# Kernel optimization log

Measured on AMD Instinct MI355X. Metric: run time of the kernel, lower is better.

The kernel has to match this reference:

```python
import jax, jax.numpy as jnp
import numpy as np

B, T, D_MODEL = 2, 1024, 512
EXPAND = 2
D_INNER = D_MODEL * EXPAND
STATE = 16
K_CONV = 4


def setup_inputs() -> dict:
    key = jax.random.key(0)
    ks = jax.random.split(key, 10)
    sc = lambda k, shape: jax.random.normal(k, shape, jnp.float32) * 0.02
    return {
        "x": jax.random.normal(ks[0], (B, T, D_MODEL), jnp.float32),
        "ln_g": jnp.ones((D_MODEL,), jnp.float32),
        "ln_b": jnp.zeros((D_MODEL,), jnp.float32),
        "W_in": sc(ks[1], (2 * D_INNER, D_MODEL)),
        "conv_w": sc(ks[2], (D_INNER, 1, K_CONV)),
        "conv_b": jnp.zeros((D_INNER,), jnp.float32),
        "W_B": sc(ks[3], (STATE, D_INNER)),
        "W_C": sc(ks[4], (STATE, D_INNER)),
        "W_dt": sc(ks[5], (D_INNER, D_INNER)),
        "b_dt": jax.random.uniform(ks[6], (D_INNER,), jnp.float32, -4.0, -1.0),
        # log_A init: A_diag = -(n+1) from HiPPO, log(-A_diag) = log(n+1), broadcast over d_inner
        "log_A": jnp.broadcast_to(jnp.log(jnp.arange(1, STATE + 1, dtype=jnp.float32)), (D_INNER, STATE)),
        "W_out": sc(ks[7], (D_MODEL, D_INNER)),
    }


def _silu(v):
    return v * jax.nn.sigmoid(v)


def reference(x, ln_g, ln_b, W_in, conv_w, conv_b, W_B, W_C, W_dt, b_dt, log_A, W_out):
    residual = x
    # LayerNorm (biased variance, eps=1e-5)
    mu = x.mean(-1, keepdims=True)
    var = x.var(-1, keepdims=True)
    xn = (x - mu) * jax.lax.rsqrt(var + 1e-5) * ln_g + ln_b
    # input projection and gate split
    xz = xn @ W_in.T                      # (B,T,2*D_INNER)
    x_main, z = jnp.split(xz, 2, axis=-1)
    # depthwise causal conv1d (padding=3 then slice to T == left-pad 3)
    xc = jnp.transpose(x_main, (0, 2, 1))  # (B,D_INNER,T)
    xc = jax.lax.conv_general_dilated(
        xc, conv_w, window_strides=(1,), padding=[(K_CONV - 1, 0)],
        dimension_numbers=("NCH", "OIH", "NCH"), feature_group_count=D_INNER,
    ) + conv_b[None, :, None]
    x_main = _silu(jnp.transpose(xc, (0, 2, 1)))  # (B,T,D_INNER)
    # selective scan in fp32
    xf = x_main.astype(jnp.float32)
    Bt = xf @ W_B.T                        # (B,T,N)
    Ct = xf @ W_C.T                        # (B,T,N)
    dt = jax.nn.softplus(xf @ W_dt.T + b_dt)  # (B,T,D_INNER)
    A = -jnp.exp(log_A)                    # (D_INNER,N)
    dA = jnp.exp(A[None, None] * dt[..., None])              # (B,T,D_INNER,N)
    dBx = dt[..., None] * Bt[:, :, None, :] * xf[..., None]  # (B,T,D_INNER,N)

    def comb(c1, c2):
        a1, b1 = c1
        a2, b2 = c2
        return a1 * a2, a2 * b1 + b2

    _, h = jax.lax.associative_scan(comb, (dA, dBx), axis=1)  # h_t = dA_t*h_{t-1}+dBx_t
    y = (h * Ct[:, :, None, :]).sum(-1).astype(x.dtype)       # (B,T,D_INNER)
    out = (y * _silu(z)) @ W_out.T
    return residual + out
```

## Files before the change

kernel.cpp:

```cpp
#include <hip/hip_runtime.h>

#define T_SEQ 1024
#define DM 512
#define DI 1024
#define NS 16
#define NC 64
#define CL 16

typedef __attribute__((ext_vector_type(8))) short short8;
typedef __attribute__((ext_vector_type(4))) float f32x4;
typedef unsigned short u16;
typedef unsigned int u32;

__device__ inline float b2f(u16 u) {
    unsigned v = ((unsigned)u) << 16;
    return __builtin_bit_cast(float, v);
}
__device__ inline u16 f2b(float f) {
    unsigned u = __builtin_bit_cast(unsigned, f);
    u += 0x7fff + ((u >> 16) & 1);
    return (u16)(u >> 16);
}

__device__ inline void g2l16(const u16* g, short* l) {
    __builtin_amdgcn_global_load_lds((const __attribute__((address_space(1))) u32*)g,
                                     (__attribute__((address_space(3))) u32*)l, 16, 0, 0);
}

__global__ void cast_w(const float* __restrict__ Win, const float* __restrict__ Wdt,
                       const float* __restrict__ Wout, const float* __restrict__ Wb,
                       const float* __restrict__ Wc,
                       u16* __restrict__ oWin, u16* __restrict__ oWdt, u16* __restrict__ oWout,
                       u16* __restrict__ oWb, u16* __restrict__ oWc) {
    int i = blockIdx.x * 256 + threadIdx.x;
    const float* s; u16* d; int off;
    if (i < 262144)      { s = Win;  d = oWin;  off = i; }
    else if (i < 524288) { s = Wdt;  d = oWdt;  off = i - 262144; }
    else if (i < 655360) { s = Wout; d = oWout; off = i - 524288; }
    else if (i < 659456) { s = Wb;   d = oWb;   off = i - 655360; }
    else                 { s = Wc;   d = oWc;   off = i - 659456; }
    float4 v = ((const float4*)s)[off];
    d[off * 4 + 0] = f2b(v.x);
    d[off * 4 + 1] = f2b(v.y);
    d[off * 4 + 2] = f2b(v.z);
    d[off * 4 + 3] = f2b(v.w);
}

__global__ __launch_bounds__(256) void ln_k(const float* __restrict__ x, const float* __restrict__ g,
                                            const float* __restrict__ be, u16* __restrict__ xn) {
    int row = blockIdx.x, tid = threadIdx.x;
    float2 v = ((const float2*)(x + row * DM))[tid];
    float s = v.x + v.y, q = v.x * v.x + v.y * v.y;
    #pragma unroll
    for (int m = 1; m < 64; m <<= 1) { s += __shfl_xor(s, m); q += __shfl_xor(q, m); }
    __shared__ float ss[4], qq[4];
    if ((tid & 63) == 0) { ss[tid >> 6] = s; qq[tid >> 6] = q; }
    __syncthreads();
    s = ss[0] + ss[1] + ss[2] + ss[3];
    q = qq[0] + qq[1] + qq[2] + qq[3];
    float mu = s / DM;
    float var = q / DM - mu * mu;
    float rs = rsqrtf(var + 1e-5f);
    int c = tid * 2;
    xn[row * DM + c]     = f2b((v.x - mu) * rs * g[c] + be[c]);
    xn[row * DM + c + 1] = f2b((v.y - mu) * rs * g[c + 1] + be[c + 1]);
}

template<int BM, int BN, int NT, int EPI>
__global__ __launch_bounds__(256) void gemm_bt(const u16* __restrict__ A, int lda,
                                               const u16* __restrict__ Bw, int ldb,
                                               void* __restrict__ outp, int ldo,
                                               const float* __restrict__ extra) {
    __shared__ short a_sh[2][BM * 32];
    __shared__ short b_sh[2][BN * 32];
    constexpr int MI = BM / 32, NJ = BN / 32;
    int tid = threadIdx.x, w = tid >> 6, lane = tid & 63;
    int m0 = blockIdx.x * BM, n0 = blockIdx.y * BN;
    int wr = (w >> 1) * (BM / 2), wc = (w & 1) * (BN / 2);
    int lr = lane & 15, kg = lane >> 4;
    f32x4 acc[MI][NJ] = {};
    const u16* Abase = A + (size_t)m0 * lda;
    const u16* Bbase = Bw + (size_t)n0 * ldb;
    int srow = w * 16 + (lane >> 2);
    int sc0 = (lane & 3);

    auto stage = [&](int cur, int kt) {
        int k0 = kt * 32;
        #pragma unroll
        for (int r = 0; r < BM / 64; ++r) {
            int row = r * 64 + srow;
            int sc = sc0 ^ ((row >> 1) & 3);
            g2l16(Abase + (size_t)row * lda + k0 + sc * 8, &a_sh[cur][r * 2048 + w * 512 + lane * 8]);
        }
        #pragma unroll
        for (int r = 0; r < BN / 64; ++r) {
            int row = r * 64 + srow;
            int sc = sc0 ^ ((row >> 1) & 3);
            g2l16(Bbase + (size_t)row * ldb + k0 + sc * 8, &b_sh[cur][r * 2048 + w * 512 + lane * 8]);
        }
    };

    stage(0, 0);
    __syncthreads();
    int cur = 0;
    for (int t = 0; t < NT; ++t) {
        if (t + 1 < NT) stage(cur ^ 1, t + 1);
        short8 af[MI], bfr[NJ];
        #pragma unroll
        for (int i = 0; i < MI; ++i) {
            int row = wr + i * 16 + lr;
            af[i] = *(const short8*)&a_sh[cur][row * 32 + (kg ^ ((row >> 1) & 3)) * 8];
        }
        #pragma unroll
        for (int j = 0; j < NJ; ++j) {
            int row = wc + j * 16 + lr;
            bfr[j] = *(const short8*)&b_sh[cur][row * 32 + (kg ^ ((row >> 1) & 3)) * 8];
        }
        #pragma unroll
        for (int i = 0; i < MI; ++i)
            #pragma unroll
            for (int j = 0; j < NJ; ++j)
                acc[i][j] = __builtin_amdgcn_mfma_f32_16x16x32_bf16(af[i], bfr[j], acc[i][j], 0, 0, 0);
        __syncthreads();
        cur ^= 1;
    }

    int rb = (lane >> 4) * 4, cc = lane & 15;
    #pragma unroll
    for (int i = 0; i < MI; ++i) {
        #pragma unroll
        for (int j = 0; j < NJ; ++j) {
            #pragma unroll
            for (int r = 0; r < 4; ++r) {
                int row = m0 + wr + i * 16 + rb + r;
                int col = n0 + wc + j * 16 + cc;
                float v = acc[i][j][r];
                if (EPI == 0) {
                    ((u16*)outp)[(size_t)row * ldo + col] = f2b(v);
                } else if (EPI == 1) {
                    float xx = v + extra[col];
                    float sp = (xx > 20.f) ? xx : log1pf(__expf(xx));
                    ((u16*)outp)[(size_t)row * ldo + col] = f2b(sp);
                } else {
                    ((float*)outp)[(size_t)row * ldo + col] = v + extra[(size_t)row * ldo + col];
                }
            }
        }
    }
}

__global__ void conv_k(const u16* __restrict__ xz, const float* __restrict__ w,
                       const float* __restrict__ cb, u16* __restrict__ xf) {
    int idx = blockIdx.x * 256 + threadIdx.x;
    int d = idx & (DI - 1);
    int bt = idx >> 10;
    int t = bt & (T_SEQ - 1);
    float s = cb[d];
    #pragma unroll
    for (int i = 0; i < 4; ++i) {
        int tt = t - 3 + i;
        if (tt >= 0) s += w[d * 4 + i] * b2f(xz[(size_t)(bt - 3 + i) * 2048 + d]);
    }
    float sig = 1.f / (1.f + __expf(-s));
    xf[idx] = f2b(s * sig);
}

__global__ __launch_bounds__(256) void bc_k(const u16* __restrict__ xf, const u16* __restrict__ Wb,
                                            const u16* __restrict__ Wc,
                                            float* __restrict__ Bt, float* __restrict__ Ct) {
    int m = blockIdx.x * 8 + (threadIdx.x >> 5);
    int j = threadIdx.x & 31;
    const u16* wrow = (j < 16) ? (Wb + j * DI) : (Wc + (j - 16) * DI);
    const short8* xr = (const short8*)(xf + (size_t)m * DI);
    const short8* wr = (const short8*)wrow;
    float s = 0.f;
    #pragma unroll 4
    for (int k = 0; k < DI / 8; ++k) {
        short8 a = xr[k], b = wr[k];
        #pragma unroll
        for (int e = 0; e < 8; ++e) s += b2f((u16)a[e]) * b2f((u16)b[e]);
    }
    float* o = (j < 16) ? Bt : Ct;
    o[(size_t)m * NS + (j & 15)] = s;
}

__global__ __launch_bounds__(256) void scanA(const u16* __restrict__ dt, const u16* __restrict__ xf,
                                             const float* __restrict__ Bt, const float* __restrict__ logA,
                                             float* __restrict__ Aprod, float* __restrict__ S) {
    int tid = threadIdx.x;
    int dblk = blockIdx.x & 3;
    int c = (blockIdx.x >> 2) & (NC - 1);
    int b = blockIdx.x >> 8;
    int d = dblk * 256 + tid;
    float Adn[NS], ap[NS], h[NS];
    #pragma unroll
    for (int j = 0; j < 4; ++j)
        *(float4*)&Adn[j * 4] = ((const float4*)(logA + (size_t)d * NS))[j];
    #pragma unroll
    for (int n = 0; n < NS; ++n) { Adn[n] = -__expf(Adn[n]); ap[n] = 1.f; h[n] = 0.f; }
    const u16* dtp = dt + ((size_t)b * T_SEQ + c * CL) * DI + d;
    const u16* xfp = xf + ((size_t)b * T_SEQ + c * CL) * DI + d;
    const float* Bp = Bt + ((size_t)b * T_SEQ + c * CL) * NS;
    #pragma unroll
    for (int i = 0; i < CL; ++i) {
        float dtv = b2f(dtp[(size_t)i * DI]);
        float xv  = b2f(xfp[(size_t)i * DI]);
        float ux = dtv * xv;
        float Bv[NS];
        #pragma unroll
        for (int j = 0; j < 4; ++j) *(float4*)&Bv[j * 4] = ((const float4*)(Bp + (size_t)i * NS))[j];
        #pragma unroll
        for (int n = 0; n < NS; ++n) {
            float dA = __expf(Adn[n] * dtv);
            h[n] = fmaf(dA, h[n], ux * Bv[n]);
            ap[n] *= dA;
        }
    }
    size_t o = ((((size_t)c * 2 + b) * DI) + d) * NS;
    #pragma unroll
    for (int j = 0; j < 4; ++j) {
        ((float4*)(Aprod + o))[j] = *(float4*)&ap[j * 4];
        ((float4*)(S + o))[j]     = *(float4*)&h[j * 4];
    }
}

__global__ __launch_bounds__(256) void scanB(const float* __restrict__ Aprod, const float* __restrict__ S,
                                             float* __restrict__ Hin) {
    int chain = blockIdx.x * 256 + threadIdx.x;
    float h = 0.f;
    #pragma unroll 8
    for (int c = 0; c < NC; ++c) {
        size_t o = (size_t)c * 32768 + chain;
        Hin[o] = h;
        h = fmaf(Aprod[o], h, S[o]);
    }
}

__global__ __launch_bounds__(256) void scanC(const u16* __restrict__ dt, const u16* __restrict__ xf,
                                             const float* __restrict__ Bt, const float* __restrict__ Ct,
                                             const float* __restrict__ logA, const float* __restrict__ Hin,
                                             const u16* __restrict__ xz, u16* __restrict__ ym) {
    int tid = threadIdx.x;
    int dblk = blockIdx.x & 3;
    int c = (blockIdx.x >> 2) & (NC - 1);
    int b = blockIdx.x >> 8;
    int d = dblk * 256 + tid;
    float Adn[NS], h[NS];
    #pragma unroll
    for (int j = 0; j < 4; ++j)
        *(float4*)&Adn[j * 4] = ((const float4*)(logA + (size_t)d * NS))[j];
    #pragma unroll
    for (int n = 0; n < NS; ++n) Adn[n] = -__expf(Adn[n]);
    size_t o = ((((size_t)c * 2 + b) * DI) + d) * NS;
    #pragma unroll
    for (int j = 0; j < 4; ++j) *(float4*)&h[j * 4] = ((const float4*)(Hin + o))[j];
    const u16* dtp = dt + ((size_t)b * T_SEQ + c * CL) * DI + d;
    const u16* xfp = xf + ((size_t)b * T_SEQ + c * CL) * DI + d;
    const float* Bp = Bt + ((size_t)b * T_SEQ + c * CL) * NS;
    const float* Cp = Ct + ((size_t)b * T_SEQ + c * CL) * NS;
    const u16* zp = xz + ((size_t)b * T_SEQ + c * CL) * 2048 + 1024 + d;
    u16* yp = ym + ((size_t)b * T_SEQ + c * CL) * DI + d;
    #pragma unroll
    for (int i = 0; i < CL; ++i) {
        float dtv = b2f(dtp[(size_t)i * DI]);
        float xv  = b2f(xfp[(size_t)i * DI]);
        float ux = dtv * xv;
        float Bv[NS], Cv[NS];
        #pragma unroll
        for (int j = 0; j < 4; ++j) {
            *(float4*)&Bv[j * 4] = ((const float4*)(Bp + (size_t)i * NS))[j];
            *(float4*)&Cv[j * 4] = ((const float4*)(Cp + (size_t)i * NS))[j];
        }
        float r = 0.f;
        #pragma unroll
        for (int n = 0; n < NS; ++n) {
            float dA = __expf(Adn[n] * dtv);
            h[n] = fmaf(dA, h[n], ux * Bv[n]);
            r = fmaf(h[n], Cv[n], r);
        }
        float zv = b2f(zp[(size_t)i * 2048]);
        float sz = zv / (1.f + __expf(-zv));
        yp[(size_t)i * DI] = f2b(r * sz);
    }
}

extern "C" void kernel_launch(void* const* d_in, const int* in_sizes, int n_in,
                              void* d_out, int out_size, void* d_ws, size_t ws_size,
                              hipStream_t stream) {
    const float* x     = (const float*)d_in[0];
    const float* ln_g  = (const float*)d_in[1];
    const float* ln_b  = (const float*)d_in[2];
    const float* W_in  = (const float*)d_in[3];
    const float* conv_w= (const float*)d_in[4];
    const float* conv_b= (const float*)d_in[5];
    const float* W_B   = (const float*)d_in[6];
    const float* W_C   = (const float*)d_in[7];
    const float* W_dt  = (const float*)d_in[8];
    const float* b_dt  = (const float*)d_in[9];
    const float* log_A = (const float*)d_in[10];
    const float* W_out = (const float*)d_in[11];

    char* ws = (char*)d_ws;
    u16* wInB  = (u16*)(ws + 0);
    u16* wDtB  = (u16*)(ws + 2097152);
    u16* wOutB = (u16*)(ws + 4194304);
    u16* wBB   = (u16*)(ws + 5242880);
    u16* wCB   = (u16*)(ws + 5275648);
    u16* xnB   = (u16*)(ws + 5308416);
    u16* xzB   = (u16*)(ws + 7405568);
    u16* xfB   = (u16*)(ws + 15794176);
    u16* dtB   = (u16*)(ws + 19988480);
    float* BtF = (float*)(ws + 24182784);
    float* CtF = (float*)(ws + 24313856);
    u16* ymB   = (u16*)(ws + 24444928);
    float* ApF = (float*)(ws + 28639232);
    float* SF  = (float*)(ws + 37027840);
    float* HiF = (float*)(ws + 45416448);

    cast_w<<<2592, 256, 0, stream>>>(W_in, W_dt, W_out, W_B, W_C, wInB, wDtB, wOutB, wBB, wCB);
    ln_k<<<2048, 256, 0, stream>>>(x, ln_g, ln_b, xnB);
    gemm_bt<128, 128, 16, 0><<<dim3(16, 16), 256, 0, stream>>>(xnB, 512, wInB, 512, (void*)xzB, 2048, nullptr);
    conv_k<<<8192, 256, 0, stream>>>(xzB, conv_w, conv_b, xfB);
    gemm_bt<128, 64, 32, 1><<<dim3(16, 16), 256, 0, stream>>>(xfB, 1024, wDtB, 1024, (void*)dtB, 1024, b_dt);
    bc_k<<<256, 256, 0, stream>>>(xfB, wBB, wCB, BtF, CtF);
    scanA<<<512, 256, 0, stream>>>(dtB, xfB, BtF, log_A, ApF, SF);
    scanB<<<128, 256, 0, stream>>>(ApF, SF, HiF);
    scanC<<<512, 256, 0, stream>>>(dtB, xfB, BtF, CtF, log_A, HiF, xzB, ymB);
    gemm_bt<64, 64, 32, 2><<<dim3(32, 8), 256, 0, stream>>>(ymB, 1024, wOutB, 1024, d_out, 512, x);
}
```

Before: 138.0 us.

## Deepen GEMM K-tile to 64, shrink block tiles, fuse weight cast with LayerNorm

The GEMM now stages 64-wide K slices per iteration, using a new 8-chunk XOR swizzle and two MFMA sub-steps per barrier. This halves the number of sync/stage iterations. Block tiles for all three GEMMs are shrunk to put more blocks on the many CUs. The weight cast and LayerNorm kernels are merged into one launch to save a kernel launch. The trade-off is more LDS per block and less operand reuse per block. The 32x64 output GEMM gives each wave only 16 rows, and the code should be checked for correctness there.

New measurement: 126.7 us. -8.1%, faster.

```diff
diff --git a/kernel.cpp b/kernel.cpp
--- a/kernel.cpp
+++ b/kernel.cpp
@@ -27,28 +27,29 @@
                                      (__attribute__((address_space(3))) u32*)l, 16, 0, 0);
 }
 
-__global__ void cast_w(const float* __restrict__ Win, const float* __restrict__ Wdt,
+__global__ __launch_bounds__(256) void prep_k(const float* __restrict__ Win, const float* __restrict__ Wdt,
                        const float* __restrict__ Wout, const float* __restrict__ Wb,
                        const float* __restrict__ Wc,
                        u16* __restrict__ oWin, u16* __restrict__ oWdt, u16* __restrict__ oWout,
-                       u16* __restrict__ oWb, u16* __restrict__ oWc) {
-    int i = blockIdx.x * 256 + threadIdx.x;
-    const float* s; u16* d; int off;
-    if (i < 262144)      { s = Win;  d = oWin;  off = i; }
-    else if (i < 524288) { s = Wdt;  d = oWdt;  off = i - 262144; }
-    else if (i < 655360) { s = Wout; d = oWout; off = i - 524288; }
-    else if (i < 659456) { s = Wb;   d = oWb;   off = i - 655360; }
-    else                 { s = Wc;   d = oWc;   off = i - 659456; }
-    float4 v = ((const float4*)s)[off];
-    d[off * 4 + 0] = f2b(v.x);
-    d[off * 4 + 1] = f2b(v.y);
-    d[off * 4 + 2] = f2b(v.z);
-    d[off * 4 + 3] = f2b(v.w);
-}
-
-__global__ __launch_bounds__(256) void ln_k(const float* __restrict__ x, const float* __restrict__ g,
-                                            const float* __restrict__ be, u16* __restrict__ xn) {
-    int row = blockIdx.x, tid = threadIdx.x;
+                       u16* __restrict__ oWb, u16* __restrict__ oWc,
+                       const float* __restrict__ x, const float* __restrict__ g,
+                       const float* __restrict__ be, u16* __restrict__ xn) {
+    if (blockIdx.x < 2592) {
+        int i = blockIdx.x * 256 + threadIdx.x;
+        const float* s; u16* d; int off;
+        if (i < 262144)      { s = Win;  d = oWin;  off = i; }
+        else if (i < 524288) { s = Wdt;  d = oWdt;  off = i - 262144; }
+        else if (i < 655360) { s = Wout; d = oWout; off = i - 524288; }
+        else if (i < 659456) { s = Wb;   d = oWb;   off = i - 655360; }
+        else                 { s = Wc;   d = oWc;   off = i - 659456; }
+        float4 v = ((const float4*)s)[off];
+        d[off * 4 + 0] = f2b(v.x);
+        d[off * 4 + 1] = f2b(v.y);
+        d[off * 4 + 2] = f2b(v.z);
+        d[off * 4 + 3] = f2b(v.w);
+        return;
+    }
+    int row = blockIdx.x - 2592, tid = threadIdx.x;
     float2 v = ((const float2*)(x + row * DM))[tid];
     float s = v.x + v.y, q = v.x * v.x + v.y * v.y;
     #pragma unroll
@@ -71,8 +72,8 @@
                                                const u16* __restrict__ Bw, int ldb,
                                                void* __restrict__ outp, int ldo,
                                                const float* __restrict__ extra) {
-    __shared__ short a_sh[2][BM * 32];
-    __shared__ short b_sh[2][BN * 32];
+    __shared__ short a_sh[2][BM * 64];
+    __shared__ short b_sh[2][BN * 64];
     constexpr int MI = BM / 32, NJ = BN / 32;
     int tid = threadIdx.x, w = tid >> 6, lane = tid & 63;
     int m0 = blockIdx.x * BM, n0 = blockIdx.y * BN;
@@ -81,22 +82,23 @@
     f32x4 acc[MI][NJ] = {};
     const u16* Abase = A + (size_t)m0 * lda;
     const u16* Bbase = Bw + (size_t)n0 * ldb;
-    int srow = w * 16 + (lane >> 2);
-    int sc0 = (lane & 3);
+    int lrow = lane >> 3;
+    int lchunk = lane & 7;
+    int schunk = lchunk ^ lrow;
 
     auto stage = [&](int cur, int kt) {
-        int k0 = kt * 32;
-        #pragma unroll
-        for (int r = 0; r < BM / 64; ++r) {
-            int row = r * 64 + srow;
-            int sc = sc0 ^ ((row >> 1) & 3);
-            g2l16(Abase + (size_t)row * lda + k0 + sc * 8, &a_sh[cur][r * 2048 + w * 512 + lane * 8]);
-        }
-        #pragma unroll
-        for (int r = 0; r < BN / 64; ++r) {
-            int row = r * 64 + srow;
-            int sc = sc0 ^ ((row >> 1) & 3);
-            g2l16(Bbase + (size_t)row * ldb + k0 + sc * 8, &b_sh[cur][r * 2048 + w * 512 + lane * 8]);
+        int k0 = kt * 64;
+        #pragma unroll
+        for (int r = 0; r < BM / 32; ++r) {
+            int row = r * 32 + w * 8 + lrow;
+            g2l16(Abase + (size_t)row * lda + k0 + schunk * 8,
+                  &a_sh[cur][(r * 32 + w * 8) * 64 + lane * 8]);
+        }
+        #pragma unroll
+        for (int r = 0; r < BN / 32; ++r) {
+            int row = r * 32 + w * 8 + lrow;
+            g2l16(Bbase + (size_t)row * ldb + k0 + schunk * 8,
+                  &b_sh[cur][(r * 32 + w * 8) * 64 + lane * 8]);
         }
     };
 
@@ -105,22 +107,25 @@
     int cur = 0;
     for (int t = 0; t < NT; ++t) {
         if (t + 1 < NT) stage(cur ^ 1, t + 1);
-        short8 af[MI], bfr[NJ];
-        #pragma unroll
-        for (int i = 0; i < MI; ++i) {
-            int row = wr + i * 16 + lr;
-            af[i] = *(const short8*)&a_sh[cur][row * 32 + (kg ^ ((row >> 1) & 3)) * 8];
-        }
-        #pragma unroll
-        for (int j = 0; j < NJ; ++j) {
-            int row = wc + j * 16 + lr;
-            bfr[j] = *(const short8*)&b_sh[cur][row * 32 + (kg ^ ((row >> 1) & 3)) * 8];
-        }
-        #pragma unroll
-        for (int i = 0; i < MI; ++i)
+        #pragma unroll
+        for (int kk = 0; kk < 2; ++kk) {
+            short8 af[MI], bfr[NJ];
             #pragma unroll
-            for (int j = 0; j < NJ; ++j)
-                acc[i][j] = __builtin_amdgcn_mfma_f32_16x16x32_bf16(af[i], bfr[j], acc[i][j], 0, 0, 0);
+            for (int i = 0; i < MI; ++i) {
+                int row = wr + i * 16 + lr;
+                af[i] = *(const short8*)&a_sh[cur][row * 64 + (((kk << 2) | kg) ^ (row & 7)) * 8];
+            }
+            #pragma unroll
+            for (int j = 0; j < NJ; ++j) {
+                int row = wc + j * 16 + lr;
+                bfr[j] = *(const short8*)&b_sh[cur][row * 64 + (((kk << 2) | kg) ^ (row & 7)) * 8];
+            }
+            #pragma unroll
+            for (int i = 0; i < MI; ++i)
+                #pragma unroll
+                for (int j = 0; j < NJ; ++j)
+                    acc[i][j] = __builtin_amdgcn_mfma_f32_16x16x32_bf16(af[i], bfr[j], acc[i][j], 0, 0, 0);
+        }
         __syncthreads();
         cur ^= 1;
     }
@@ -317,14 +322,14 @@
     float* SF  = (float*)(ws + 37027840);
     float* HiF = (float*)(ws + 45416448);
 
-    cast_w<<<2592, 256, 0, stream>>>(W_in, W_dt, W_out, W_B, W_C, wInB, wDtB, wOutB, wBB, wCB);
-    ln_k<<<2048, 256, 0, stream>>>(x, ln_g, ln_b, xnB);
-    gemm_bt<128, 128, 16, 0><<<dim3(16, 16), 256, 0, stream>>>(xnB, 512, wInB, 512, (void*)xzB, 2048, nullptr);
+    prep_k<<<4640, 256, 0, stream>>>(W_in, W_dt, W_out, W_B, W_C, wInB, wDtB, wOutB, wBB, wCB,
+                                     x, ln_g, ln_b, xnB);
+    gemm_bt<64, 64, 8, 0><<<dim3(32, 32), 256, 0, stream>>>(xnB, 512, wInB, 512, (void*)xzB, 2048, nullptr);
     conv_k<<<8192, 256, 0, stream>>>(xzB, conv_w, conv_b, xfB);
-    gemm_bt<128, 64, 32, 1><<<dim3(16, 16), 256, 0, stream>>>(xfB, 1024, wDtB, 1024, (void*)dtB, 1024, b_dt);
+    gemm_bt<64, 64, 16, 1><<<dim3(32, 16), 256, 0, stream>>>(xfB, 1024, wDtB, 1024, (void*)dtB, 1024, b_dt);
     bc_k<<<256, 256, 0, stream>>>(xfB, wBB, wCB, BtF, CtF);
     scanA<<<512, 256, 0, stream>>>(dtB, xfB, BtF, log_A, ApF, SF);
     scanB<<<128, 256, 0, stream>>>(ApF, SF, HiF);
     scanC<<<512, 256, 0, stream>>>(dtB, xfB, BtF, CtF, log_A, HiF, xzB, ymB);
-    gemm_bt<64, 64, 32, 2><<<dim3(32, 8), 256, 0, stream>>>(ymB, 1024, wOutB, 1024, d_out, 512, x);
-}
+    gemm_bt<32, 64, 16, 2><<<dim3(64, 8), 256, 0, stream>>>(ymB, 1024, wOutB, 1024, d_out, 512, x);
+}
```
